# Optimization experiments

Measured on AMD Instinct MI355X. Metric: run time of the kernel, lower is better.

## Reference

```python
import jax, jax.numpy as jnp
import numpy as np

H, N, L, BATCH = 128, 64, 4096, 8


def _make_dplr_hippo(n):
    # HiPPO-LegS -> NPLR -> DPLR diagonalization (float64 numpy, as in torch source)
    ar = np.arange(n, dtype=np.float64)
    p0 = np.sqrt(1.0 + 2.0 * ar)
    A = p0[:, None] * p0[None, :]
    A = np.tril(A) - np.diag(ar)
    nhippo = -A
    Pv = np.sqrt(ar + 0.5)
    Bv = np.sqrt(2.0 * ar + 1.0)
    S = nhippo + Pv[:, None] * Pv[None, :]
    Lambda_real = np.mean(np.diag(S)) * np.ones(n)
    Lambda_imag, V = np.linalg.eigh(S * -1j)
    V = V.astype(np.complex64)
    P = (V.conj().T @ Pv.astype(np.complex64))
    B = (V.conj().T @ Bv.astype(np.complex64))
    Lam = (Lambda_real + 1j * Lambda_imag).astype(np.complex64)
    return Lam, P, B


def _ri(x):  # complex -> [..., 2] real view (like torch.view_as_real)
    return np.stack([x.real, x.imag], axis=-1).astype(np.float32)


def setup_inputs() -> dict:
    key = jax.random.key(0)
    k_u, k_c, k_d = jax.random.split(key, 3)
    Lam, P, B = _make_dplr_hippo(N)
    Lambda_ri = np.tile(_ri(Lam)[None], (H, 1, 1))          # [H, N, 2]
    P_ri = np.tile(_ri(P)[None], (H, 1, 1))                 # [H, N, 2]
    B_ri = np.tile(_ri(B)[None], (H, 1, 1))                 # [H, N, 2]
    C_ri = jax.random.normal(k_c, (H, N, 2), dtype=jnp.float32)
    D = jax.random.normal(k_d, (H, 1), dtype=jnp.float32)
    u = jax.random.normal(k_u, (BATCH, L, H), dtype=jnp.float32)
    step = jnp.array([1.0 / L], dtype=jnp.float32)
    return {
        "u": u,
        "B_ri": jnp.asarray(B_ri),
        "C_ri": jnp.asarray(C_ri),
        "D": D,
        "Lambda_ri": jnp.asarray(Lambda_ri),
        "P_ri": jnp.asarray(P_ri),
        "step": step,
    }


def _as_c(x_ri):
    return jax.lax.complex(x_ri[..., 0], x_ri[..., 1])


def reference(u, B_ri, C_ri, D, Lambda_ri, P_ri, step):
    Bc = _as_c(B_ri)        # [H, N] complex64
    Cc = _as_c(C_ri)        # [H, N]
    Lam = _as_c(Lambda_ri)  # [H, N]
    Pc = _as_c(P_ri)        # [H, N]
    batch, seq_len, h = u.shape

    # roots of unity and bilinear-transform terms
    z = jnp.exp(-2j * jnp.pi * jnp.arange(seq_len) / seq_len)   # [L] complex64
    g = (2.0 / step).astype(jnp.complex64) * ((1.0 - z) / (1.0 + z))  # [L]
    c = 2.0 / (1.0 + z)                                          # [L]

    # Cauchy resolvent, shared by the four cauchy_dot reductions: [H, L, N]
    r = 1.0 / (g[None, :, None] - Lam[:, None, :])

    def cauchy(v):  # v: [H, N] -> [H, L]
        return jnp.einsum("hn,hln->hl", v, r)

    k00 = cauchy(jnp.conj(Cc) * Bc)
    k01 = cauchy(jnp.conj(Cc) * Pc)
    k10 = cauchy(jnp.conj(Pc) * Bc)
    k11 = cauchy(jnp.conj(Pc) * Pc)
    at_roots = c[None, :] * (k00 - k01 * (1.0 / (1.0 + k11)) * k10)  # [H, L]

    kernel = jnp.fft.ifft(at_roots, n=seq_len, axis=-1).real  # [H, L] float32

    # linear (full) FFT convolution, length 2L-1, keep first L samples
    nfft = 2 * seq_len - 1
    u_f = jnp.fft.rfft(u, n=nfft, axis=1)                 # [B, F, H]
    k_f = jnp.fft.rfft(kernel, n=nfft, axis=-1)           # [H, F]
    y = jnp.fft.irfft(u_f * k_f.T[None], n=nfft, axis=1)[:, :seq_len, :]  # [B, L, H]

    return y + u @ D  # D: [H,1] -> broadcast add of skip term
```

## Files before the change

kernel.cpp:

```cpp
#include <hip/hip_runtime.h>
#include <hip/hip_bf16.h>
#include <math.h>

#define HH 128
#define NN 64
#define LL 4096
#define BB 8
#define NFFT 8192
#define KSTR 4160

#define CAU_BLOCKS 2048
#define TRU_BLOCKS 4096
#define SKP_BLOCKS 8192

__device__ __forceinline__ float2 cmul(float2 a, float2 b) {
    return make_float2(a.x * b.x - a.y * b.y, a.x * b.y + a.y * b.x);
}
__device__ __forceinline__ float2 cadd(float2 a, float2 b) {
    return make_float2(a.x + b.x, a.y + b.y);
}
__device__ __forceinline__ float2 csub(float2 a, float2 b) {
    return make_float2(a.x - b.x, a.y - b.y);
}
__device__ __forceinline__ int brev13(int x) { return (int)(__brev((unsigned)x) >> 19); }
__device__ __forceinline__ int kkmap(int t) {
    return (t < 4096) ? (((t & 63) << 6) | (t >> 6)) : 4096;
}

__device__ __forceinline__ float2 twid(float rev, float sg) {
    return make_float2(__builtin_amdgcn_cosf(rev), sg * __builtin_amdgcn_sinf(rev));
}


template <int M>
__device__ __forceinline__ void dif_f4(float2* d, int N, int tid, int nt, float sg) {
    const float inv2m = 1.0f / (2.0f * (float)M);
    const float inv4m = 1.0f / (4.0f * (float)M);
    for (int q = tid; q < (N >> 2); q += nt) {
        int j = q & (M - 1);
        int i0 = ((q & ~(M - 1)) << 2) + j;
        float2 x0 = d[i0], x1 = d[i0 + M], x2 = d[i0 + 2 * M], x3 = d[i0 + 3 * M];
        float jf = (float)j;
        float2 wB = twid(jf * inv4m, sg);
        float2 wA = twid(jf * inv2m, sg);
        float2 a0 = cadd(x0, x2);
        float2 a2 = cmul(wB, csub(x0, x2));
        float2 a1 = cadd(x1, x3);
        float2 t = cmul(wB, csub(x1, x3));
        float2 a3 = make_float2(-sg * t.y, sg * t.x);
        d[i0] = cadd(a0, a1);
        d[i0 + M] = cmul(wA, csub(a0, a1));
        d[i0 + 2 * M] = cadd(a2, a3);
        d[i0 + 3 * M] = cmul(wA, csub(a2, a3));
    }
    __syncthreads();
}

template <int M>
__device__ __forceinline__ void dit_f4(float2* d, int N, int tid, int nt, float sg) {
    const float inv2m = 1.0f / (2.0f * (float)M);
    const float inv4m = 1.0f / (4.0f * (float)M);
    for (int q = tid; q < (N >> 2); q += nt) {
        int j = q & (M - 1);
        int i0 = ((q & ~(M - 1)) << 2) + j;
        float2 x0 = d[i0], x1 = d[i0 + M], x2 = d[i0 + 2 * M], x3 = d[i0 + 3 * M];
        float jf = (float)j;
        float2 wA = twid(jf * inv2m, sg);
        float2 wB = twid(jf * inv4m, sg);
        float2 t0 = cmul(wA, x1), t1 = cmul(wA, x3);
        float2 a0 = cadd(x0, t0), a1 = csub(x0, t0);
        float2 a2 = cadd(x2, t1), a3 = csub(x2, t1);
        float2 u = cmul(wB, a2), v = cmul(wB, a3);
        float2 vi = make_float2(-sg * v.y, sg * v.x);
        d[i0] = cadd(a0, u);
        d[i0 + 2 * M] = csub(a0, u);
        d[i0 + M] = cadd(a1, vi);
        d[i0 + 3 * M] = csub(a1, vi);
    }
    __syncthreads();
}

__global__ __launch_bounds__(256) void stage1_kernel(
    const float* __restrict__ u,
    const float* __restrict__ B_ri, const float* __restrict__ C_ri,
    const float* __restrict__ D,
    const float* __restrict__ Lambda_ri, const float* __restrict__ P_ri,
    const float* __restrict__ step,
    float2* __restrict__ at_g, float* __restrict__ ut, float* __restrict__ skip) {
    __shared__ float4 smem[272];
    const int bid = blockIdx.x;
    const int tid = threadIdx.x;

    if (bid < CAU_BLOCKS) {
        float4* tabA = smem;
        float4* tabB = smem + 64;
        float2* tabC = (float2*)(smem + 128);
        const int h = bid >> 4;
        if (tid < NN) {
            int n = tid;
            float2 C = ((const float2*)C_ri)[h * NN + n];
            float2 Bv = ((const float2*)B_ri)[h * NN + n];
            float2 P = ((const float2*)P_ri)[h * NN + n];
            float2 lam = ((const float2*)Lambda_ri)[h * NN + n];
            float2 Cc = make_float2(C.x, -C.y);
            float2 Pc = make_float2(P.x, -P.y);
            float2 v00 = cmul(Cc, Bv);
            float2 v01 = cmul(Cc, P);
            float2 v10 = cmul(Pc, Bv);
            float2 v11 = cmul(Pc, P);
            tabA[n] = make_float4(lam.x, lam.y, v00.x, v00.y);
            tabB[n] = make_float4(v01.x, v01.y, v10.x, v10.y);
            tabC[n] = v11;
        }
        __syncthreads();

        const int l = ((bid & 15) << 8) | tid;
        const float two_over_step = 2.0f / step[0];
        double th = -6.283185307179586476925286766559 * (double)l / (double)LL;
        float sn, cs;
        sincosf((float)th, &sn, &cs);
        float dr = 1.0f + cs, di = sn;
        float inv = __builtin_amdgcn_rcpf(dr * dr + di * di);
        float nr = 1.0f - cs, ni = -sn;
        float gr = two_over_step * (nr * dr + ni * di) * inv;
        float gi = two_over_step * (ni * dr - nr * di) * inv;
        float2 cc = make_float2(2.0f * dr * inv, -2.0f * di * inv);

        float2 k00 = make_float2(0.f, 0.f), k01 = make_float2(0.f, 0.f);
        float2 k10 = make_float2(0.f, 0.f), k11 = make_float2(0.f, 0.f);
#pragma unroll 8
        for (int n = 0; n < NN; ++n) {
            float4 tA = tabA[n];
            float4 tB = tabB[n];
            float2 tC = tabC[n];
            float ar = gr - tA.x, ai = gi - tA.y;
            float id = __builtin_amdgcn_rcpf(ar * ar + ai * ai);
            float2 r = make_float2(ar * id, -ai * id);
            k00 = cadd(k00, cmul(make_float2(tA.z, tA.w), r));
            k01 = cadd(k01, cmul(make_float2(tB.x, tB.y), r));
            k10 = cadd(k10, cmul(make_float2(tB.z, tB.w), r));
            k11 = cadd(k11, cmul(tC, r));
        }
        float wr = 1.0f + k11.x, wi = k11.y;
        float iw = __builtin_amdgcn_rcpf(wr * wr + wi * wi);
        float2 winv = make_float2(wr * iw, -wi * iw);
        float2 t = cmul(cmul(k01, winv), k10);
        float2 at = cmul(cc, make_float2(k00.x - t.x, k00.y - t.y));
        at_g[(size_t)h * LL + l] = at;
    } else if (bid < CAU_BLOCKS + TRU_BLOCKS) {
        float* tile = (float*)smem;
        int tb = bid - CAU_BLOCKS;
        int b = tb >> 9;
        int h0 = ((tb >> 7) & 3) * 32;
        int l0 = (tb & 127) * 32;
        int tx = tid & 31, ty = tid >> 5;
        const float* up = u + (size_t)b * LL * HH;
        float* utp = ut + (size_t)b * HH * LL;
        for (int i = ty; i < 32; i += 8)
            tile[i * 33 + tx] = up[(size_t)(l0 + i) * HH + h0 + tx];
        __syncthreads();
        for (int i = ty; i < 32; i += 8)
            utp[(size_t)(h0 + i) * LL + l0 + tx] = tile[tx * 33 + i];
    } else {
        int sb = bid - (CAU_BLOCKS + TRU_BLOCKS);
        int wid = tid >> 6, lane = tid & 63;
        int row = sb * 4 + wid;
        const float* ur = u + (size_t)row * HH;
        float v = ur[lane] * D[lane] + ur[lane + 64] * D[lane + 64];
        for (int off = 32; off > 0; off >>= 1) v += __shfl_down(v, off, 64);
        if (lane == 0) skip[row] = v;
    }
}

__global__ __launch_bounds__(1024) void kfreq_kernel(const float2* __restrict__ at_g,
                                                     float2* __restrict__ KfP) {
    __shared__ float2 sm[NFFT];
    const int h = blockIdx.x;
    const int tid = threadIdx.x;
    const float2* ap = at_g + (size_t)h * LL;
#pragma unroll
    for (int it = 0; it < 4; ++it) {
        int t = tid + it * 1024;
        int l = ((t & 63) << 6) | (t >> 6);
        sm[__brev((unsigned)l) >> 20] = ap[l];
    }
    __syncthreads();

    dit_f4<1>(sm, 4096, tid, 1024, +1.f);
    dit_f4<4>(sm, 4096, tid, 1024, +1.f);
    dit_f4<16>(sm, 4096, tid, 1024, +1.f);
    dit_f4<64>(sm, 4096, tid, 1024, +1.f);
    dit_f4<256>(sm, 4096, tid, 1024, +1.f);
    dit_f4<1024>(sm, 4096, tid, 1024, +1.f);

    const float inv8192 = 1.0f / 8192.0f;
    for (int t = tid; t < 4096; t += 1024) {
        float kv = sm[t].x * (1.0f / 4096.0f);
        float2 w = twid((float)t * inv8192, -1.f);
        sm[t] = make_float2(kv, 0.f);
        sm[t + 4096] = make_float2(kv * w.x, kv * w.y);
    }
    __syncthreads();

    dif_f4<1024>(sm, 8192, tid, 1024, -1.f);
    dif_f4<256>(sm, 8192, tid, 1024, -1.f);
    dif_f4<64>(sm, 8192, tid, 1024, -1.f);
    dif_f4<16>(sm, 8192, tid, 1024, -1.f);
    dif_f4<4>(sm, 8192, tid, 1024, -1.f);
    dif_f4<1>(sm, 8192, tid, 1024, -1.f);

    float2* kfp = KfP + (size_t)h * KSTR;
    for (int t = tid; t <= 4096; t += 1024) kfp[t] = sm[brev13(kkmap(t))];
}

__global__ __launch_bounds__(1024) void conv_fft_kernel(const float* __restrict__ ut,
                                                        const float2* __restrict__ KfP,
                                                        float* __restrict__ yt) {
    __shared__ float2 sm[NFFT];
    const int b = blockIdx.x >> 6;
    const int c = blockIdx.x & 63;
    const int h0 = 2 * c, h1 = 2 * c + 1;
    const int tid = threadIdx.x;
    const float* up0 = ut + ((size_t)b * HH + h0) * LL;
    const float* up1 = ut + ((size_t)b * HH + h1) * LL;
    const float inv8192 = 1.0f / 8192.0f;

    for (int i = tid; i < 4096; i += 1024) {
        float2 a = make_float2(up0[i], up1[i]);
        float2 w = twid((float)i * inv8192, -1.f);
        sm[i] = a;
        sm[i + 4096] = cmul(w, a);
    }
    __syncthreads();

    dif_f4<1024>(sm, 8192, tid, 1024, -1.f);
    dif_f4<256>(sm, 8192, tid, 1024, -1.f);
    dif_f4<64>(sm, 8192, tid, 1024, -1.f);
    dif_f4<16>(sm, 8192, tid, 1024, -1.f);
    dif_f4<4>(sm, 8192, tid, 1024, -1.f);
    dif_f4<1>(sm, 8192, tid, 1024, -1.f);

    const float2* kf0 = KfP + (size_t)h0 * KSTR;
    const float2* kf1 = KfP + (size_t)h1 * KSTR;
    for (int t = tid; t <= 4096; t += 1024) {
        int kk = kkmap(t);
        bool self = (kk == 0) || (kk == 4096);
        int p = brev13(kk);
        int q = self ? p : brev13(NFFT - kk);
        float2 K0 = kf0[t];
        float2 K1 = kf1[t];
        float2 Zp = sm[p];
        float2 Zq = sm[q];
        float2 U0 = make_float2(0.5f * (Zp.x + Zq.x), 0.5f * (Zp.y - Zq.y));
        float2 U1 = make_float2(0.5f * (Zp.y + Zq.y), 0.5f * (Zq.x - Zp.x));
        float2 A = cmul(U0, K0);
        float2 C = cmul(U1, K1);
        sm[p] = make_float2(A.x - C.y, A.y + C.x);
        if (!self) sm[q] = make_float2(A.x + C.y, C.x - A.y);
    }
    __syncthreads();

    dit_f4<1>(sm, 8192, tid, 1024, +1.f);
    dit_f4<4>(sm, 8192, tid, 1024, +1.f);
    dit_f4<16>(sm, 8192, tid, 1024, +1.f);
    dit_f4<64>(sm, 8192, tid, 1024, +1.f);
    dit_f4<256>(sm, 8192, tid, 1024, +1.f);
    dit_f4<1024>(sm, 8192, tid, 1024, +1.f);

    float* yp0 = yt + ((size_t)b * HH + h0) * LL;
    float* yp1 = yt + ((size_t)b * HH + h1) * LL;
    const float invN = 1.0f / (float)NFFT;
    for (int x = tid; x < 4096; x += 1024) {
        float2 w = twid((float)x * inv8192, +1.f);
        float2 a = sm[x];
        float2 bb = cmul(w, sm[x + 4096]);
        yp0[x] = (a.x + bb.x) * invN;
        yp1[x] = (a.y + bb.y) * invN;
    }
}

__global__ __launch_bounds__(256) void transpose_y_kernel(const float* __restrict__ yt,
                                                          const float* __restrict__ skip,
                                                          float* __restrict__ y) {
    __shared__ float tile[32][33];
    int b = blockIdx.z;
    int h0 = blockIdx.x * 32, l0 = blockIdx.y * 32;
    const float* ytp = yt + (size_t)b * HH * LL;
    const float* skp = skip + (size_t)b * LL;
    float* yp = y + (size_t)b * LL * HH;
    for (int i = threadIdx.y; i < 32; i += 8)
        tile[i][threadIdx.x] = ytp[(size_t)(h0 + i) * LL + l0 + threadIdx.x];
    __syncthreads();
    for (int i = threadIdx.y; i < 32; i += 8) {
        size_t idx = (size_t)(l0 + i) * HH + h0 + threadIdx.x;
        yp[idx] = tile[threadIdx.x][i] + skp[l0 + i];
    }
}

extern "C" void kernel_launch(void* const* d_in, const int* in_sizes, int n_in,
                              void* d_out, int out_size, void* d_ws, size_t ws_size,
                              hipStream_t stream) {
    const float* u = (const float*)d_in[0];
    const float* B_ri = (const float*)d_in[1];
    const float* C_ri = (const float*)d_in[2];
    const float* D = (const float*)d_in[3];
    const float* Lambda_ri = (const float*)d_in[4];
    const float* P_ri = (const float*)d_in[5];
    const float* step = (const float*)d_in[6];
    float* out = (float*)d_out;

    char* ws = (char*)d_ws;
    float2* KfP = (float2*)ws;
    float* skip = (float*)(ws + (size_t)6 * 1024 * 1024);
    float* ut = (float*)(ws + (size_t)8 * 1024 * 1024);
    float* yt = (float*)(ws + (size_t)24 * 1024 * 1024);
    float2* at_g = (float2*)yt;

    stage1_kernel<<<dim3(CAU_BLOCKS + TRU_BLOCKS + SKP_BLOCKS), dim3(256), 0, stream>>>(
        u, B_ri, C_ri, D, Lambda_ri, P_ri, step, at_g, ut, skip);
    kfreq_kernel<<<dim3(HH), dim3(1024), 0, stream>>>(at_g, KfP);
    conv_fft_kernel<<<dim3(BB * HH / 2), dim3(1024), 0, stream>>>(ut, KfP, yt);
    transpose_y_kernel<<<dim3(HH / 32, LL / 32, BB), dim3(32, 8), 0, stream>>>(yt, skip, out);
}
```

Measured before the change: 93.56 us.

## Precompute Cauchy tables in separate kernel and interleave stage1 block roles

```diff
diff --git a/kernel.cpp b/kernel.cpp
--- a/kernel.cpp
+++ b/kernel.cpp
@@ -8,10 +8,6 @@
 #define BB 8
 #define NFFT 8192
 #define KSTR 4160
-
-#define CAU_BLOCKS 2048
-#define TRU_BLOCKS 4096
-#define SKP_BLOCKS 8192
 
 __device__ __forceinline__ float2 cmul(float2 a, float2 b) {
     return make_float2(a.x * b.x - a.y * b.y, a.x * b.y + a.y * b.x);
@@ -80,41 +76,43 @@
     __syncthreads();
 }
 
+__global__ __launch_bounds__(512) void tabgen_kernel(
+    const float* __restrict__ B_ri, const float* __restrict__ C_ri,
+    const float* __restrict__ Lambda_ri, const float* __restrict__ P_ri,
+    float4* __restrict__ tabAB, float2* __restrict__ tabC) {
+    int i = blockIdx.x * 512 + threadIdx.x;
+    float2 C = ((const float2*)C_ri)[i];
+    float2 Bv = ((const float2*)B_ri)[i];
+    float2 P = ((const float2*)P_ri)[i];
+    float2 lam = ((const float2*)Lambda_ri)[i];
+    float2 Cc = make_float2(C.x, -C.y);
+    float2 Pc = make_float2(P.x, -P.y);
+    float2 v00 = cmul(Cc, Bv);
+    float2 v01 = cmul(Cc, P);
+    float2 v10 = cmul(Pc, Bv);
+    float2 v11 = cmul(Pc, P);
+    tabAB[2 * i] = make_float4(lam.x, lam.y, v00.x, v00.y);
+    tabAB[2 * i + 1] = make_float4(v01.x, v01.y, v10.x, v10.y);
+    tabC[i] = v11;
+}
+
 __global__ __launch_bounds__(256) void stage1_kernel(
-    const float* __restrict__ u,
-    const float* __restrict__ B_ri, const float* __restrict__ C_ri,
-    const float* __restrict__ D,
-    const float* __restrict__ Lambda_ri, const float* __restrict__ P_ri,
+    const float* __restrict__ u, const float* __restrict__ D,
+    const float4* __restrict__ tabAB, const float2* __restrict__ tabC,
     const float* __restrict__ step,
     float2* __restrict__ at_g, float* __restrict__ ut, float* __restrict__ skip) {
-    __shared__ float4 smem[272];
+    __shared__ float tile[32 * 33];
     const int bid = blockIdx.x;
     const int tid = threadIdx.x;
-
-    if (bid < CAU_BLOCKS) {
-        float4* tabA = smem;
-        float4* tabB = smem + 64;
-        float2* tabC = (float2*)(smem + 128);
-        const int h = bid >> 4;
-        if (tid < NN) {
-            int n = tid;
-            float2 C = ((const float2*)C_ri)[h * NN + n];
-            float2 Bv = ((const float2*)B_ri)[h * NN + n];
-            float2 P = ((const float2*)P_ri)[h * NN + n];
-            float2 lam = ((const float2*)Lambda_ri)[h * NN + n];
-            float2 Cc = make_float2(C.x, -C.y);
-            float2 Pc = make_float2(P.x, -P.y);
-            float2 v00 = cmul(Cc, Bv);
-            float2 v01 = cmul(Cc, P);
-            float2 v10 = cmul(Pc, Bv);
-            float2 v11 = cmul(Pc, P);
-            tabA[n] = make_float4(lam.x, lam.y, v00.x, v00.y);
-            tabB[n] = make_float4(v01.x, v01.y, v10.x, v10.y);
-            tabC[n] = v11;
-        }
-        __syncthreads();
-
-        const int l = ((bid & 15) << 8) | tid;
+    const int part = bid % 7;
+    const int sub = bid / 7;
+
+    if (part == 0) {
+        const int h = sub >> 4;
+        const float4* tA = tabAB + (size_t)(h * NN) * 2;
+        const float2* tC = tabC + (size_t)h * NN;
+
+        const int l = ((sub & 15) << 8) | tid;
         const float two_over_step = 2.0f / step[0];
         double th = -6.283185307179586476925286766559 * (double)l / (double)LL;
         float sn, cs;
@@ -130,16 +128,16 @@
         float2 k10 = make_float2(0.f, 0.f), k11 = make_float2(0.f, 0.f);
 #pragma unroll 8
         for (int n = 0; n < NN; ++n) {
-            float4 tA = tabA[n];
-            float4 tB = tabB[n];
-            float2 tC = tabC[n];
-            float ar = gr - tA.x, ai = gi - tA.y;
+            float4 tAv = tA[2 * n];
+            float4 tBv = tA[2 * n + 1];
+            float2 tCv = tC[n];
+            float ar = gr - tAv.x, ai = gi - tAv.y;
             float id = __builtin_amdgcn_rcpf(ar * ar + ai * ai);
             float2 r = make_float2(ar * id, -ai * id);
-            k00 = cadd(k00, cmul(make_float2(tA.z, tA.w), r));
-            k01 = cadd(k01, cmul(make_float2(tB.x, tB.y), r));
-            k10 = cadd(k10, cmul(make_float2(tB.z, tB.w), r));
-            k11 = cadd(k11, cmul(tC, r));
+            k00 = cadd(k00, cmul(make_float2(tAv.z, tAv.w), r));
+            k01 = cadd(k01, cmul(make_float2(tBv.x, tBv.y), r));
+            k10 = cadd(k10, cmul(make_float2(tBv.z, tBv.w), r));
+            k11 = cadd(k11, cmul(tCv, r));
         }
         float wr = 1.0f + k11.x, wi = k11.y;
         float iw = __builtin_amdgcn_rcpf(wr * wr + wi * wi);
@@ -147,9 +145,8 @@
         float2 t = cmul(cmul(k01, winv), k10);
         float2 at = cmul(cc, make_float2(k00.x - t.x, k00.y - t.y));
         at_g[(size_t)h * LL + l] = at;
-    } else if (bid < CAU_BLOCKS + TRU_BLOCKS) {
-        float* tile = (float*)smem;
-        int tb = bid - CAU_BLOCKS;
+    } else if (part <= 2) {
+        int tb = sub * 2 + (part - 1);
         int b = tb >> 9;
         int h0 = ((tb >> 7) & 3) * 32;
         int l0 = (tb & 127) * 32;
@@ -162,7 +159,7 @@
         for (int i = ty; i < 32; i += 8)
             utp[(size_t)(h0 + i) * LL + l0 + tx] = tile[tx * 33 + i];
     } else {
-        int sb = bid - (CAU_BLOCKS + TRU_BLOCKS);
+        int sb = sub * 4 + (part - 3);
         int wid = tid >> 6, lane = tid & 63;
         int row = sb * 4 + wid;
         const float* ur = u + (size_t)row * HH;
@@ -311,13 +308,15 @@
 
     char* ws = (char*)d_ws;
     float2* KfP = (float2*)ws;
+    float4* tabAB = (float4*)(ws + (size_t)5 * 1024 * 1024);
+    float2* tabC = (float2*)(ws + (size_t)5 * 1024 * 1024 + 384 * 1024);
     float* skip = (float*)(ws + (size_t)6 * 1024 * 1024);
     float* ut = (float*)(ws + (size_t)8 * 1024 * 1024);
     float* yt = (float*)(ws + (size_t)24 * 1024 * 1024);
     float2* at_g = (float2*)yt;
 
-    stage1_kernel<<<dim3(CAU_BLOCKS + TRU_BLOCKS + SKP_BLOCKS), dim3(256), 0, stream>>>(
-        u, B_ri, C_ri, D, Lambda_ri, P_ri, step, at_g, ut, skip);
+    tabgen_kernel<<<dim3(16), dim3(512), 0, stream>>>(B_ri, C_ri, Lambda_ri, P_ri, tabAB, tabC);
+    stage1_kernel<<<dim3(7 * 2048), dim3(256), 0, stream>>>(u, D, tabAB, tabC, step, at_g, ut, skip);
     kfreq_kernel<<<dim3(HH), dim3(1024), 0, stream>>>(at_g, KfP);
     conv_fft_kernel<<<dim3(BB * HH / 2), dim3(1024), 0, stream>>>(ut, KfP, yt);
     transpose_y_kernel<<<dim3(HH / 32, LL / 32, BB), dim3(32, 8), 0, stream>>>(yt, skip, out);
```

After: 107.4 us. +14.8%, slower.
